# Optimization experiments

Hardware: AMD Instinct MI355X
Metric: run time of the kernel (lower is better)

## Reference

```python
import jax, jax.numpy as jnp
import numpy as np

B, SMAX, TMAX, D = 8, 4096, 4096, 528


def setup_inputs() -> dict:
    key = jax.random.key(0)
    ks = jax.random.split(key, 20)
    src_lens = (np.arange(B) * 256 + 2048).astype(np.int64)  # 2048..3840, sum 23552
    tgt_lens = (np.arange(B) * 224 + 2304).astype(np.int64)  # 2304..3872, sum 24704
    Ns, Nt = int(src_lens.sum()), int(tgt_lens.sum())
    N = Ns + Nt  # 48256 packed coarse points (src then tgt)
    src_mask = jnp.asarray(np.arange(SMAX)[None, :] < src_lens[:, None])
    tgt_mask = jnp.asarray(np.arange(TMAX)[None, :] < tgt_lens[:, None])
    sics = np.concatenate([b * SMAX + np.arange(l) for b, l in enumerate(src_lens)])
    tics = np.concatenate([b * TMAX + np.arange(l) for b, l in enumerate(tgt_lens)])
    w = lambda k, shape: (jax.random.normal(k, shape, jnp.float32) * 0.02)
    return dict(
        geo_feats=jax.random.normal(ks[0], (N, D), jnp.float32),
        pcd=jax.random.normal(ks[1], (N, 3), jnp.float32),
        Wi1=w(ks[2], (528, 528)), bi1=w(ks[3], (528,)),
        Wi2=w(ks[4], (1024, 528)), bi2=w(ks[5], (1024,)),
        Wc1=w(ks[6], (528, 528)), bc1=w(ks[7], (528,)),
        Wc2=w(ks[8], (1024, 528)), bc2=w(ks[9], (1024,)),
        Ws1=w(ks[10], (512, 2576)), bs1=w(ks[11], (512,)),
        Ws2=w(ks[12], (256, 512)), bs2=w(ks[13], (256,)),
        Ws3=w(ks[14], (1, 256)), bs3=w(ks[15], (1,)),
        src_mask=src_mask, tgt_mask=tgt_mask,
        src_ind_coarse_split=jnp.asarray(sics, jnp.int32),
        tgt_ind_coarse_split=jnp.asarray(tics, jnp.int32),
        src_ind_coarse=jnp.arange(Ns, dtype=jnp.int32),
        tgt_ind_coarse=Ns + jnp.arange(Nt, dtype=jnp.int32),
    )


def _scatter(vals, flat_idx, b, n, d):
    # split_feats: zeros[b*n, d]; out[flat_idx] = vals; view(b, n, d)
    return jnp.zeros((b * n, d), vals.dtype).at[flat_idx].set(vals).reshape(b, n, d)


def _pw(x, W, b):
    # pointwise Conv1d(in->out, k=1) as a batched matmul over positions
    return jnp.einsum('bnd,od->bno', x, W) + b


def reference(geo_feats, pcd, Wi1, bi1, Wi2, bi2, Wc1, bc1, Wc2, bc2,
              Ws1, bs1, Ws2, bs2, Ws3, bs3,
              src_mask, tgt_mask, src_ind_coarse_split, tgt_ind_coarse_split,
              src_ind_coarse, tgt_ind_coarse):
    b, smax = src_mask.shape
    tmax = tgt_mask.shape[1]
    d = geo_feats.shape[-1]

    # split_feats: ragged gather -> padded [B, pts_max, D]
    src_feats = _scatter(geo_feats[src_ind_coarse], src_ind_coarse_split, b, smax, d)
    tgt_feats = _scatter(geo_feats[tgt_ind_coarse], tgt_ind_coarse_split, b, tmax, d)
    s_pcd = _scatter(pcd[src_ind_coarse], src_ind_coarse_split, b, smax, 3)
    t_pcd = _scatter(pcd[tgt_ind_coarse], tgt_ind_coarse_split, b, tmax, 3)

    sm = src_mask.astype(src_feats.dtype)
    tm = tgt_mask.astype(tgt_feats.dtype)

    # inst_global over valid src points (per-sample slice -> masked mean)
    h = jax.nn.relu(_pw(src_feats, Wi1, bi1))
    h = jax.nn.relu(_pw(h, Wi2, bi2))                      # [B, Smax, 1024]
    inst_g = jnp.einsum('bno,bn->bo', h, sm) / sm.sum(1, keepdims=True)

    # category_global over valid tgt points
    g = jax.nn.relu(_pw(tgt_feats, Wc1, bc1))
    g = jax.nn.relu(_pw(g, Wc2, bc2))                      # [B, Tmax, 1024]
    cat_g = jnp.einsum('bno,bn->bo', g, tm) / tm.sum(1, keepdims=True)

    # scale_net on concat(src_feats, inst_g, cat_g) without materializing [B,N,2576]:
    # split first conv weight over the concat axis; globals contribute per-batch constants
    Ws1_s, Ws1_i, Ws1_c = Ws1[:, :d], Ws1[:, d:d + 1024], Ws1[:, d + 1024:]
    glob = inst_g @ Ws1_i.T + cat_g @ Ws1_c.T + bs1        # [B, 512]
    z = jax.nn.relu(jnp.einsum('bnd,od->bno', src_feats, Ws1_s) + glob[:, None, :])
    z = jax.nn.relu(_pw(z, Ws2, bs2))                      # [B, Smax, 256]
    s = _pw(z, Ws3, bs3)                                   # [B, Smax, 1]
    scale_mat = jax.nn.sigmoid(s).transpose(0, 2, 1) - 0.5  # [B, 1, Smax]

    inv = 1.0 / jnp.sqrt(jnp.asarray(d, src_feats.dtype))
    return (src_feats * inv, tgt_feats * inv, s_pcd, t_pcd, scale_mat)
```

## Files before the change

### kernel.cpp

```cpp
#include <hip/hip_runtime.h>
#include <hip/hip_bf16.h>
#include <cstdint>
#include <cstddef>

typedef float f32x4 __attribute__((ext_vector_type(4)));
typedef __bf16 bf16x8v __attribute__((ext_vector_type(8)));
typedef __hip_bfloat16 bf16;

__device__ __forceinline__ void gld16(const void* g, void* l) {
  __builtin_amdgcn_global_load_lds((const __attribute__((address_space(1))) void*)g,
                                   (__attribute__((address_space(3))) void*)l, 16, 0, 0);
}


struct PrepP {
  const float* Wsrc[6];
  bf16* Wdst[6];
  int sld[6], rows[6], K[6], Kpad[6];
  int off[10];
  float* zbuf; int ztotal;
  const float* geo; bf16* geo_b; int Nrows;
  const int* sics; const int* tics; int Ns, Nt; int* cnt;
};

__global__ void prep_kernel(PrepP P) {
  int blk = blockIdx.x;
  int job = 0;
  while (job < 8 && blk >= P.off[job + 1]) ++job;
  int local = blk - P.off[job];
  if (job < 6) {
    int i = local * 256 + threadIdx.x;
    int kp = P.Kpad[job];
    int total = P.rows[job] * kp;
    if (i < total) {
      int r = i / kp, k = i - r * kp;
      float v = (k < P.K[job]) ? P.Wsrc[job][(size_t)r * P.sld[job] + k] : 0.f;
      P.Wdst[job][i] = __float2bfloat16(v);
    }
  } else if (job == 6) {
    int i = local * 256 + threadIdx.x;
    if (i < P.ztotal) P.zbuf[i] = 0.f;
  } else if (job == 7) {
    int t = local * 256 + threadIdx.x;
    int row = t / 72, c8 = t - row * 72;
    if (row < P.Nrows) {
      int col = c8 * 8;
      bf16* dst = P.geo_b + (size_t)row * 576 + col;
      if (c8 < 66) {
        const float* s = P.geo + (size_t)row * 528 + col;
        float4 f0 = ((const float4*)s)[0], f1 = ((const float4*)s)[1];
        bf16 h[8] = {__float2bfloat16(f0.x), __float2bfloat16(f0.y),
                     __float2bfloat16(f0.z), __float2bfloat16(f0.w),
                     __float2bfloat16(f1.x), __float2bfloat16(f1.y),
                     __float2bfloat16(f1.z), __float2bfloat16(f1.w)};
        ((uint4*)dst)[0] = *(uint4*)h;
      } else {
        uint4 z = {0u, 0u, 0u, 0u};
        ((uint4*)dst)[0] = z;
      }
    }
  } else {
    int j = local * 256 + threadIdx.x;
    if (j < P.Ns) {
      if (j == 0) { P.cnt[0] = 0; P.cnt[8] = P.Ns; }
      else { int b = P.sics[j] >> 12; if ((P.sics[j - 1] >> 12) != b) P.cnt[b] = j; }
    }
    if (j < P.Nt) {
      if (j == 0) { P.cnt[9] = 0; P.cnt[17] = P.Nt; }
      else { int b = P.tics[j] >> 12; if ((P.tics[j - 1] >> 12) != b) P.cnt[9 + b] = j; }
    }
  }
}

__device__ __forceinline__ void gemm_core(
    const bf16* __restrict__ Aptr, int lda,
    const bf16* __restrict__ Bw, int ldb,
    int m0, int n0, int kiters,
    bf16* __restrict__ lA, bf16* __restrict__ lB,
    f32x4 acc[4][4])
{
  const int tid  = threadIdx.x;
  const int lane = tid & 63;
  const int quad = lane >> 4;
  const int l16  = lane & 15;
  const int wr   = tid >> 7;
  const int wc   = (tid >> 6) & 1;
  const int srow = tid >> 2;
  const int scol = (tid & 3) << 3;
  const bf16* aA0 = Aptr + (size_t)(m0 + srow) * lda + scol;
  const bf16* aA1 = aA0 + (size_t)64 * lda;
  const bf16* aB0 = Bw + (size_t)(n0 + srow) * ldb + scol;
  const bf16* aB1 = aB0 + (size_t)64 * ldb;
  bf16* lA00 = lA + tid * 8;        bf16* lA01 = lA + 2048 + tid * 8;
  bf16* lA10 = lA + 4096 + tid * 8; bf16* lA11 = lA + 6144 + tid * 8;
  bf16* lB00 = lB + tid * 8;        bf16* lB01 = lB + 2048 + tid * 8;
  bf16* lB10 = lB + 4096 + tid * 8; bf16* lB11 = lB + 6144 + tid * 8;

  for (int k = 0; k < kiters; ++k) {
    const int k0 = k * 64;
    gld16(aA0 + k0, lA00);      gld16(aA1 + k0, lA01);
    gld16(aA0 + k0 + 32, lA10); gld16(aA1 + k0 + 32, lA11);
    gld16(aB0 + k0, lB00);      gld16(aB1 + k0, lB01);
    gld16(aB0 + k0 + 32, lB10); gld16(aB1 + k0 + 32, lB11);
    __syncthreads();
#pragma unroll
    for (int kk = 0; kk < 2; ++kk) {
      bf16x8v af[4], bfr[4];
#pragma unroll
      for (int i = 0; i < 4; ++i) {
        af[i]  = *(const bf16x8v*)&lA[kk * 4096 + (wr * 64 + i * 16 + l16) * 32 + quad * 8];
        bfr[i] = *(const bf16x8v*)&lB[kk * 4096 + (wc * 64 + i * 16 + l16) * 32 + quad * 8];
      }
#pragma unroll
      for (int mi = 0; mi < 4; ++mi)
#pragma unroll
        for (int ni = 0; ni < 4; ++ni)
          acc[mi][ni] = __builtin_amdgcn_mfma_f32_16x16x32_bf16(af[mi], bfr[ni], acc[mi][ni], 0, 0, 0);
    }
    __syncthreads();
  }
}

__global__ __launch_bounds__(256, 2)
void kernelA(const bf16* __restrict__ geo_b,
             const bf16* __restrict__ Wi1b, const bf16* __restrict__ Wc1b,
             const bf16* __restrict__ Ws1sb,
             const float* __restrict__ bi1, const float* __restrict__ bc1,
             bf16* __restrict__ big_s, bf16* __restrict__ big_t,
             bf16* __restrict__ zpre, int Ms, int Mt)
{
  __shared__ alignas(16) bf16 lA[8192], lB[8192];
  const int x = blockIdx.x;
  const int e0 = Ms * 5, e1 = e0 + Mt * 5;
  const bf16 *A, *B; const float* bias = nullptr; bf16* out;
  int m0, n0, ldo, epi;
  if (x < e0) {
    int mt = x / 5, nt = x - mt * 5;
    m0 = mt * 128; n0 = nt * 128;
    A = geo_b; B = Wi1b; bias = bi1; out = big_s; ldo = 576; epi = 0;
  } else if (x < e1) {
    int y = x - e0; int mt = y / 5, nt = y - mt * 5;
    m0 = mt * 128; n0 = nt * 128;
    A = geo_b + (size_t)Ms * 128 * 576; B = Wc1b; bias = bc1; out = big_t; ldo = 576; epi = 0;
  } else {
    int y = x - e1; int mt = y / 4, nt = y - mt * 4;
    m0 = mt * 128; n0 = nt * 128;
    A = geo_b; B = Ws1sb; out = zpre; ldo = 512; epi = 1;
  }

  f32x4 acc[4][4];
  const f32x4 z4 = {0.f, 0.f, 0.f, 0.f};
#pragma unroll
  for (int i = 0; i < 4; ++i)
#pragma unroll
    for (int j = 0; j < 4; ++j) acc[i][j] = z4;

  gemm_core(A, 576, B, 576, m0, n0, 9, lA, lB, acc);

  const int lane = threadIdx.x & 63, quad = lane >> 4, l16 = lane & 15;
  const int wr = threadIdx.x >> 7, wc = (threadIdx.x >> 6) & 1;
#pragma unroll
  for (int mi = 0; mi < 4; ++mi) {
#pragma unroll
    for (int r = 0; r < 4; ++r) {
      const int row = m0 + wr * 64 + mi * 16 + quad * 4 + r;
#pragma unroll
      for (int ni = 0; ni < 4; ++ni) {
        const int col = n0 + wc * 64 + ni * 16 + l16;
        if (epi == 0) {
          if (col < 528)
            out[(size_t)row * ldo + col] = __float2bfloat16(fmaxf(acc[mi][ni][r] + bias[col], 0.f));
          else if (col < 576)
            out[(size_t)row * ldo + col] = __float2bfloat16(0.f);
        } else {
          out[(size_t)row * ldo + col] = __float2bfloat16(acc[mi][ni][r]);
        }
      }
    }
  }
}

__global__ __launch_bounds__(256, 2)
void kernelB(const bf16* __restrict__ big_s, const bf16* __restrict__ big_t,
             const bf16* __restrict__ Wi2b, const bf16* __restrict__ Wc2b,
             const float* __restrict__ bi2, const float* __restrict__ bc2,
             float* __restrict__ iacc, float* __restrict__ cacc,
             const int* __restrict__ sics, const int* __restrict__ tics,
             int Ms, int Mt,
             const float* __restrict__ geo, const float* __restrict__ pcd,
             const int* __restrict__ cnt,
             float* __restrict__ out0, float* __restrict__ out1,
             float* __restrict__ out2, float* __restrict__ out3,
             int Ns, float inv)
{
  __shared__ alignas(16) bf16 lA[8192], lB[8192];
  const int x = blockIdx.x;
  const int e0 = Ms * 8, e1 = e0 + Mt * 8;
  if (x >= e1) {
    int f = x - e1;
    int lane = threadIdx.x & 63;
    int rv = f * 4 + (threadIdx.x >> 6);
    bool is_t = rv >= 32768;
    int pos = is_t ? rv - 32768 : rv;
    int b = pos >> 12, r = pos & 4095;
    int base = is_t ? cnt[9 + b] : cnt[b];
    int lim  = (is_t ? cnt[9 + b + 1] : cnt[b + 1]) - base;
    float* op = (is_t ? out1 : out0) + (size_t)pos * 528;
    float* pp = (is_t ? out3 : out2) + (size_t)pos * 3;
    if (r < lim) {
      int sr = (is_t ? Ns : 0) + base + r;
      const float4* g = (const float4*)(geo + (size_t)sr * 528);
      for (int d = lane; d < 132; d += 64) {
        float4 v = g[d];
        float4 s = {v.x * inv, v.y * inv, v.z * inv, v.w * inv};
        ((float4*)op)[d] = s;
      }
      if (lane < 3) pp[lane] = pcd[(size_t)sr * 3 + lane];
    } else {
      float4 z = {0.f, 0.f, 0.f, 0.f};
      for (int d = lane; d < 132; d += 64) ((float4*)op)[d] = z;
      if (lane < 3) pp[lane] = 0.f;
    }
    return;
  }
  const bf16 *A, *B; const float* bias; float* red; const int* ridx;
  int m0, n0;
  if (x < e0) {
    int mt = x / 8, nt = x - mt * 8;
    m0 = mt * 128; n0 = nt * 128;
    A = big_s; B = Wi2b; bias = bi2; red = iacc; ridx = sics;
  } else {
    int y = x - e0; int mt = y / 8, nt = y - mt * 8;
    m0 = mt * 128; n0 = nt * 128;
    A = big_t; B = Wc2b; bias = bc2; red = cacc; ridx = tics;
  }

  f32x4 acc[4][4];
  const f32x4 z4 = {0.f, 0.f, 0.f, 0.f};
#pragma unroll
  for (int i = 0; i < 4; ++i)
#pragma unroll
    for (int j = 0; j < 4; ++j) acc[i][j] = z4;

  gemm_core(A, 576, B, 576, m0, n0, 9, lA, lB, acc);

  const int lane = threadIdx.x & 63, quad = lane >> 4, l16 = lane & 15;
  const int wr = threadIdx.x >> 7, wc = (threadIdx.x >> 6) & 1;
  const int b0r = ridx[m0] >> 12;
#pragma unroll
  for (int ni = 0; ni < 4; ++ni) {
    const int col = n0 + wc * 64 + ni * 16 + l16;
    const float bcol = bias[col];
#pragma unroll
    for (int mi = 0; mi < 4; ++mi) {
      float v0 = 0.f, v1 = 0.f;
#pragma unroll
      for (int r = 0; r < 4; ++r) {
        const int row = m0 + wr * 64 + mi * 16 + quad * 4 + r;
        const float v = fmaxf(acc[mi][ni][r] + bcol, 0.f);
        const int b = ridx[row] >> 12;
        if (b == b0r) v0 += v; else v1 += v;
      }
      v0 += __shfl_xor(v0, 16, 64); v0 += __shfl_xor(v0, 32, 64);
      v1 += __shfl_xor(v1, 16, 64); v1 += __shfl_xor(v1, 32, 64);
      if (quad == 0) {
        atomicAdd(&red[b0r * 1024 + col], v0);
        if (b0r + 1 < 8 && v1 != 0.f) atomicAdd(&red[(b0r + 1) * 1024 + col], v1);
      }
    }
  }
}

__global__ __launch_bounds__(256, 2)
void kernelC(const bf16* __restrict__ zpre, const bf16* __restrict__ Ws2b,
             const float* __restrict__ bs2, const float* __restrict__ Ws3,
             float* __restrict__ sbuf)
{
  __shared__ alignas(16) bf16 lA[8192], lB[8192];
  const int m0 = blockIdx.x * 128, n0 = blockIdx.y * 128;
  f32x4 acc[4][4];
  const f32x4 z4 = {0.f, 0.f, 0.f, 0.f};
#pragma unroll
  for (int i = 0; i < 4; ++i)
#pragma unroll
    for (int j = 0; j < 4; ++j) acc[i][j] = z4;

  gemm_core(zpre, 512, Ws2b, 512, m0, n0, 8, lA, lB, acc);

  const int lane = threadIdx.x & 63, quad = lane >> 4, l16 = lane & 15;
  const int wr = threadIdx.x >> 7, wc = (threadIdx.x >> 6) & 1;
#pragma unroll
  for (int mi = 0; mi < 4; ++mi) {
#pragma unroll
    for (int r = 0; r < 4; ++r) {
      const int row = m0 + wr * 64 + mi * 16 + quad * 4 + r;
      float p = 0.f;
#pragma unroll
      for (int ni = 0; ni < 4; ++ni) {
        const int col = n0 + wc * 64 + ni * 16 + l16;
        p += fmaxf(acc[mi][ni][r] + bs2[col], 0.f) * Ws3[col];
      }
      p += __shfl_xor(p, 1, 64); p += __shfl_xor(p, 2, 64);
      p += __shfl_xor(p, 4, 64); p += __shfl_xor(p, 8, 64);
      if (l16 == 0) atomicAdd(&sbuf[row], p);
    }
  }
}

__global__ __launch_bounds__(256) void glob_kernel(const float* __restrict__ iacc,
                                                   const float* __restrict__ cacc,
                                                   const int* __restrict__ cnt,
                                                   const float* __restrict__ Ws1,
                                                   const float* __restrict__ bs1,
                                                   float* __restrict__ globv) {
  int w    = (blockIdx.x * 256 + threadIdx.x) >> 6;
  int lane = threadIdx.x & 63;
  int b = w >> 9;
  int o = w & 511;
  const float* wi  = Ws1 + (size_t)o * 2576 + 528;
  const float* wcp = Ws1 + (size_t)o * 2576 + 1552;
  float a1 = 0.f, a2 = 0.f;
  for (int k = lane; k < 1024; k += 64) {
    a1 += iacc[b * 1024 + k] * wi[k];
    a2 += cacc[b * 1024 + k] * wcp[k];
  }
  for (int off = 32; off; off >>= 1) {
    a1 += __shfl_xor(a1, off, 64);
    a2 += __shfl_xor(a2, off, 64);
  }
  if (lane == 0) {
    float ns = (float)(cnt[b + 1] - cnt[b]);
    float nt = (float)(cnt[9 + b + 1] - cnt[9 + b]);
    globv[b * 512 + o] = bs1[o] + a1 / ns + a2 / nt;
  }
}

__global__ __launch_bounds__(256) void s_empty_kernel(const float* __restrict__ globv,
                                                      const float* __restrict__ Ws2,
                                                      const float* __restrict__ bs2,
                                                      const float* __restrict__ Ws3,
                                                      const float* __restrict__ bs3,
                                                      float* __restrict__ semp) {
  __shared__ float zrow[512];
  __shared__ float wsum[4];
  int b = blockIdx.x, t = threadIdx.x;
  zrow[t]       = fmaxf(globv[b * 512 + t], 0.f);
  zrow[t + 256] = fmaxf(globv[b * 512 + t + 256], 0.f);
  __syncthreads();
  float acc = bs2[t];
  for (int o = 0; o < 512; ++o) acc += zrow[o] * Ws2[t * 512 + o];
  float p = fmaxf(acc, 0.f) * Ws3[t];
  for (int off = 32; off; off >>= 1) p += __shfl_xor(p, off, 64);
  if ((t & 63) == 0) wsum[t >> 6] = p;
  __syncthreads();
  if (t == 0) semp[b] = wsum[0] + wsum[1] + wsum[2] + wsum[3] + bs3[0];
}

__global__ void zfix_kernel(bf16* __restrict__ z, const float* __restrict__ globv,
                            const int* __restrict__ sics, int total) {
  int idx = blockIdx.x * 256 + threadIdx.x;
  if (idx >= total) return;
  int row = idx >> 6, c0 = (idx & 63) << 3;
  int b = sics[row] >> 12;
  const float* gv = globv + b * 512 + c0;
  bf16* zp = z + (size_t)row * 512 + c0;
  uint4 u = *(uint4*)zp;
  bf16* e = (bf16*)&u;
#pragma unroll
  for (int i = 0; i < 8; ++i)
    e[i] = __float2bfloat16(fmaxf(__bfloat162float(e[i]) + gv[i], 0.f));
  *(uint4*)zp = u;
}

__global__ void scale_kernel(const float* __restrict__ sbuf,
                             const float* __restrict__ semp,
                             const int* __restrict__ cnt,
                             const float* __restrict__ bs3,
                             float* __restrict__ out4) {
  int i = blockIdx.x * 256 + threadIdx.x;
  if (i >= 32768) return;
  int b = i >> 12, r = i & 4095;
  int base = cnt[b];
  int lim = cnt[b + 1] - base;
  float s = (r < lim) ? sbuf[base + r] + bs3[0] : semp[b];
  out4[i] = 1.f / (1.f + expf(-s)) - 0.5f;
}


extern "C" void kernel_launch(void* const* d_in, const int* in_sizes, int n_in,
                              void* d_out, int out_size, void* d_ws, size_t ws_size,
                              hipStream_t stream) {
  const float* geo = (const float*)d_in[0];
  const float* pcd = (const float*)d_in[1];
  const float* Wi1 = (const float*)d_in[2];
  const float* bi1 = (const float*)d_in[3];
  const float* Wi2 = (const float*)d_in[4];
  const float* bi2 = (const float*)d_in[5];
  const float* Wc1 = (const float*)d_in[6];
  const float* bc1 = (const float*)d_in[7];
  const float* Wc2 = (const float*)d_in[8];
  const float* bc2 = (const float*)d_in[9];
  const float* Ws1 = (const float*)d_in[10];
  const float* bs1 = (const float*)d_in[11];
  const float* Ws2 = (const float*)d_in[12];
  const float* bs2 = (const float*)d_in[13];
  const float* Ws3 = (const float*)d_in[14];
  const float* bs3 = (const float*)d_in[15];
  const int* sics = (const int*)d_in[18];
  const int* tics = (const int*)d_in[19];
  const int Ns = in_sizes[18];
  const int Nt = in_sizes[19];
  const int Ms = Ns / 128, Mt = Nt / 128;
  const int Nrows = Ns + Nt;

  float* out0 = (float*)d_out;
  float* out1 = out0 + (size_t)8 * 4096 * 528;
  float* out2 = out1 + (size_t)8 * 4096 * 528;
  float* out3 = out2 + (size_t)8 * 4096 * 3;
  float* out4 = out3 + (size_t)8 * 4096 * 3;

  char* wp = (char*)d_ws;
  auto alloc = [&](size_t bytes) -> void* {
    void* p = (void*)wp;
    wp += (bytes + 255) & ~(size_t)255;
    return p;
  };
  int*   cnt   = (int*)  alloc(128);
  float* iacc  = (float*)alloc((size_t)8 * 1024 * 4);
  float* cacc  = (float*)alloc((size_t)8 * 1024 * 4);
  float* sbuf  = (float*)alloc((size_t)Ns * 4);
  float* globb = (float*)alloc((size_t)8 * 512 * 4);
  float* semp  = (float*)alloc(64);
  bf16* Wi1b  = (bf16*)alloc((size_t)640  * 576 * 2);
  bf16* Wi2b  = (bf16*)alloc((size_t)1024 * 576 * 2);
  bf16* Wc1b  = (bf16*)alloc((size_t)640  * 576 * 2);
  bf16* Wc2b  = (bf16*)alloc((size_t)1024 * 576 * 2);
  bf16* Ws1sb = (bf16*)alloc((size_t)512  * 576 * 2);
  bf16* Ws2b  = (bf16*)alloc((size_t)256  * 512 * 2);
  bf16* geo_b = (bf16*)alloc((size_t)Nrows * 576 * 2);
  bf16* big_s = (bf16*)alloc((size_t)Ns * 576 * 2);
  bf16* big_t = (bf16*)alloc((size_t)Nt * 576 * 2);
  bf16* zpre  = (bf16*)alloc((size_t)Ns * 512 * 2);

  PrepP P;
  {
    const float* srcs[6] = {Wi1, Wi2, Wc1, Wc2, Ws1, Ws2};
    bf16* dsts[6]        = {Wi1b, Wi2b, Wc1b, Wc2b, Ws1sb, Ws2b};
    int slds[6] = {528, 528, 528, 528, 2576, 512};
    int rows[6] = {528, 1024, 528, 1024, 512, 256};
    int Ks[6]   = {528, 528, 528, 528, 528, 512};
    int Kps[6]  = {576, 576, 576, 576, 576, 512};
    int nblk = 0;
    for (int i = 0; i < 6; ++i) {
      P.Wsrc[i] = srcs[i]; P.Wdst[i] = dsts[i]; P.sld[i] = slds[i];
      P.rows[i] = rows[i]; P.K[i] = Ks[i]; P.Kpad[i] = Kps[i];
      P.off[i] = nblk;
      nblk += (rows[i] * Kps[i] + 255) / 256;
    }
    P.off[6] = nblk;
    P.zbuf = iacc; P.ztotal = 8192 + 8192 + Ns;
    nblk += (P.ztotal + 255) / 256;
    P.off[7] = nblk;
    P.geo = geo; P.geo_b = geo_b; P.Nrows = Nrows;
    nblk += ((Nrows * 72) + 255) / 256;
    P.off[8] = nblk;
    P.sics = sics; P.tics = tics; P.Ns = Ns; P.Nt = Nt; P.cnt = cnt;
    int n = Ns > Nt ? Ns : Nt;
    nblk += (n + 255) / 256;
    P.off[9] = nblk;
    prep_kernel<<<dim3(nblk), dim3(256), 0, stream>>>(P);
  }

  kernelA<<<dim3(Ms * 5 + Mt * 5 + Ms * 4), dim3(256), 0, stream>>>(
      geo_b, Wi1b, Wc1b, Ws1sb, bi1, bc1, big_s, big_t, zpre, Ms, Mt);

  float inv = 1.0f / sqrtf(528.0f);
  kernelB<<<dim3(Ms * 8 + Mt * 8 + 16384), dim3(256), 0, stream>>>(
      big_s, big_t, Wi2b, Wc2b, bi2, bc2, iacc, cacc, sics, tics, Ms, Mt,
      geo, pcd, cnt, out0, out1, out2, out3, Ns, inv);

  glob_kernel<<<dim3(1024), dim3(256), 0, stream>>>(iacc, cacc, cnt, Ws1, bs1, globb);
  s_empty_kernel<<<dim3(8), dim3(256), 0, stream>>>(globb, Ws2, bs2, Ws3, bs3, semp);
  zfix_kernel<<<dim3((Ns * 64 + 255) / 256), dim3(256), 0, stream>>>(zpre, globb, sics, Ns * 64);
  kernelC<<<dim3(Ms, 2), dim3(256), 0, stream>>>(zpre, Ws2b, bs2, Ws3, sbuf);
  scale_kernel<<<dim3(128), dim3(256), 0, stream>>>(sbuf, semp, cnt, bs3, out4);
}
```

Before: 518.2 us.

## Fuse scaled-feature scatter into prep pass and add XCD-aware block swizzle

Moves the scaled feature and point-cloud scatter out of kernelB's extra blocks into the prep kernel's bf16 conversion pass. geo is now read once for both the bf16 copy and the scaled fp32 output, and only padding rows are zeroed, found by binary search. It also remaps block indices in kernelA, kernelB and kernelC so consecutive tiles stay on the same XCD for L2 reuse. The cost is an index lookup per prep thread and somewhat scattered writes.

```diff
diff --git a/kernel.cpp b/kernel.cpp
--- a/kernel.cpp
+++ b/kernel.cpp
@@ -12,21 +12,35 @@
                                    (__attribute__((address_space(3))) void*)l, 16, 0, 0);
 }
 
+__device__ __forceinline__ int xcd_swz(int orig, int nwg) {
+  int q = nwg >> 3, r = nwg & 7;
+  int x = orig & 7, i = orig >> 3;
+  return (x < r ? x * (q + 1) : r * (q + 1) + (x - r) * q) + i;
+}
+
+__device__ __forceinline__ int lbound(const int* a, int n, int v) {
+  int lo = 0, hi = n;
+  while (lo < hi) { int m = (lo + hi) >> 1; if (a[m] < v) lo = m + 1; else hi = m; }
+  return lo;
+}
+
 
 struct PrepP {
   const float* Wsrc[6];
   bf16* Wdst[6];
   int sld[6], rows[6], K[6], Kpad[6];
-  int off[10];
+  int off[11];
   float* zbuf; int ztotal;
   const float* geo; bf16* geo_b; int Nrows;
+  const float* pcd;
+  float* out0; float* out1; float* out2; float* out3; float inv;
   const int* sics; const int* tics; int Ns, Nt; int* cnt;
 };
 
 __global__ void prep_kernel(PrepP P) {
   int blk = blockIdx.x;
   int job = 0;
-  while (job < 8 && blk >= P.off[job + 1]) ++job;
+  while (job < 9 && blk >= P.off[job + 1]) ++job;
   int local = blk - P.off[job];
   if (job < 6) {
     int i = local * 256 + threadIdx.x;
@@ -44,6 +58,8 @@
     int t = local * 256 + threadIdx.x;
     int row = t / 72, c8 = t - row * 72;
     if (row < P.Nrows) {
+      bool is_t = row >= P.Ns;
+      int pos = is_t ? P.tics[row - P.Ns] : P.sics[row];
       int col = c8 * 8;
       bf16* dst = P.geo_b + (size_t)row * 576 + col;
       if (c8 < 66) {
@@ -54,12 +70,21 @@
                      __float2bfloat16(f1.x), __float2bfloat16(f1.y),
                      __float2bfloat16(f1.z), __float2bfloat16(f1.w)};
         ((uint4*)dst)[0] = *(uint4*)h;
+        float* op = (is_t ? P.out1 : P.out0) + (size_t)pos * 528 + col;
+        float4 s0 = {f0.x * P.inv, f0.y * P.inv, f0.z * P.inv, f0.w * P.inv};
+        float4 s1 = {f1.x * P.inv, f1.y * P.inv, f1.z * P.inv, f1.w * P.inv};
+        ((float4*)op)[0] = s0;
+        ((float4*)op)[1] = s1;
       } else {
         uint4 z = {0u, 0u, 0u, 0u};
         ((uint4*)dst)[0] = z;
+        if (c8 < 69) {
+          int j = c8 - 66;
+          (is_t ? P.out3 : P.out2)[(size_t)pos * 3 + j] = P.pcd[(size_t)row * 3 + j];
+        }
       }
     }
-  } else {
+  } else if (job == 8) {
     int j = local * 256 + threadIdx.x;
     if (j < P.Ns) {
       if (j == 0) { P.cnt[0] = 0; P.cnt[8] = P.Ns; }
@@ -68,6 +93,22 @@
     if (j < P.Nt) {
       if (j == 0) { P.cnt[9] = 0; P.cnt[17] = P.Nt; }
       else { int b = P.tics[j] >> 12; if ((P.tics[j - 1] >> 12) != b) P.cnt[9 + b] = j; }
+    }
+  } else {
+    int lane = threadIdx.x & 63;
+    int rv = local * 4 + (threadIdx.x >> 6);
+    bool is_t = rv >= 32768;
+    int pos = is_t ? rv - 32768 : rv;
+    int b = pos >> 12, r = pos & 4095;
+    const int* arr = is_t ? P.tics : P.sics;
+    int n = is_t ? P.Nt : P.Ns;
+    int lo = lbound(arr, n, b << 12);
+    int hi = lbound(arr, n, (b + 1) << 12);
+    if (r >= hi - lo) {
+      float* op = (is_t ? P.out1 : P.out0) + (size_t)pos * 528;
+      float4 z = {0.f, 0.f, 0.f, 0.f};
+      for (int d = lane; d < 132; d += 64) ((float4*)op)[d] = z;
+      if (lane < 3) (is_t ? P.out3 : P.out2)[(size_t)pos * 3 + lane] = 0.f;
     }
   }
 }
@@ -130,7 +171,7 @@
              bf16* __restrict__ zpre, int Ms, int Mt)
 {
   __shared__ alignas(16) bf16 lA[8192], lB[8192];
-  const int x = blockIdx.x;
+  const int x = xcd_swz(blockIdx.x, gridDim.x);
   const int e0 = Ms * 5, e1 = e0 + Mt * 5;
   const bf16 *A, *B; const float* bias = nullptr; bf16* out;
   int m0, n0, ldo, epi;
@@ -186,43 +227,11 @@
              const float* __restrict__ bi2, const float* __restrict__ bc2,
              float* __restrict__ iacc, float* __restrict__ cacc,
              const int* __restrict__ sics, const int* __restrict__ tics,
-             int Ms, int Mt,
-             const float* __restrict__ geo, const float* __restrict__ pcd,
-             const int* __restrict__ cnt,
-             float* __restrict__ out0, float* __restrict__ out1,
-             float* __restrict__ out2, float* __restrict__ out3,
-             int Ns, float inv)
+             int Ms, int Mt)
 {
   __shared__ alignas(16) bf16 lA[8192], lB[8192];
-  const int x = blockIdx.x;
-  const int e0 = Ms * 8, e1 = e0 + Mt * 8;
-  if (x >= e1) {
-    int f = x - e1;
-    int lane = threadIdx.x & 63;
-    int rv = f * 4 + (threadIdx.x >> 6);
-    bool is_t = rv >= 32768;
-    int pos = is_t ? rv - 32768 : rv;
-    int b = pos >> 12, r = pos & 4095;
-    int base = is_t ? cnt[9 + b] : cnt[b];
-    int lim  = (is_t ? cnt[9 + b + 1] : cnt[b + 1]) - base;
-    float* op = (is_t ? out1 : out0) + (size_t)pos * 528;
-    float* pp = (is_t ? out3 : out2) + (size_t)pos * 3;
-    if (r < lim) {
-      int sr = (is_t ? Ns : 0) + base + r;
-      const float4* g = (const float4*)(geo + (size_t)sr * 528);
-      for (int d = lane; d < 132; d += 64) {
-        float4 v = g[d];
-        float4 s = {v.x * inv, v.y * inv, v.z * inv, v.w * inv};
-        ((float4*)op)[d] = s;
-      }
-      if (lane < 3) pp[lane] = pcd[(size_t)sr * 3 + lane];
-    } else {
-      float4 z = {0.f, 0.f, 0.f, 0.f};
-      for (int d = lane; d < 132; d += 64) ((float4*)op)[d] = z;
-      if (lane < 3) pp[lane] = 0.f;
-    }
-    return;
-  }
+  const int x = xcd_swz(blockIdx.x, gridDim.x);
+  const int e0 = Ms * 8;
   const bf16 *A, *B; const float* bias; float* red; const int* ridx;
   int m0, n0;
   if (x < e0) {
@@ -277,7 +286,8 @@
              float* __restrict__ sbuf)
 {
   __shared__ alignas(16) bf16 lA[8192], lB[8192];
-  const int m0 = blockIdx.x * 128, n0 = blockIdx.y * 128;
+  const int x = xcd_swz(blockIdx.x, gridDim.x);
+  const int m0 = (x >> 1) * 128, n0 = (x & 1) * 128;
   f32x4 acc[4][4];
   const f32x4 z4 = {0.f, 0.f, 0.f, 0.f};
 #pragma unroll
@@ -442,6 +452,8 @@
   bf16* big_t = (bf16*)alloc((size_t)Nt * 576 * 2);
   bf16* zpre  = (bf16*)alloc((size_t)Ns * 512 * 2);
 
+  float inv = 1.0f / sqrtf(528.0f);
+
   PrepP P;
   {
     const float* srcs[6] = {Wi1, Wi2, Wc1, Wc2, Ws1, Ws2};
@@ -462,26 +474,28 @@
     nblk += (P.ztotal + 255) / 256;
     P.off[7] = nblk;
     P.geo = geo; P.geo_b = geo_b; P.Nrows = Nrows;
+    P.pcd = pcd;
+    P.out0 = out0; P.out1 = out1; P.out2 = out2; P.out3 = out3; P.inv = inv;
     nblk += ((Nrows * 72) + 255) / 256;
     P.off[8] = nblk;
     P.sics = sics; P.tics = tics; P.Ns = Ns; P.Nt = Nt; P.cnt = cnt;
     int n = Ns > Nt ? Ns : Nt;
     nblk += (n + 255) / 256;
     P.off[9] = nblk;
+    nblk += 65536 / 4;
+    P.off[10] = nblk;
     prep_kernel<<<dim3(nblk), dim3(256), 0, stream>>>(P);
   }
 
   kernelA<<<dim3(Ms * 5 + Mt * 5 + Ms * 4), dim3(256), 0, stream>>>(
       geo_b, Wi1b, Wc1b, Ws1sb, bi1, bc1, big_s, big_t, zpre, Ms, Mt);
 
-  float inv = 1.0f / sqrtf(528.0f);
-  kernelB<<<dim3(Ms * 8 + Mt * 8 + 16384), dim3(256), 0, stream>>>(
-      big_s, big_t, Wi2b, Wc2b, bi2, bc2, iacc, cacc, sics, tics, Ms, Mt,
-      geo, pcd, cnt, out0, out1, out2, out3, Ns, inv);
+  kernelB<<<dim3(Ms * 8 + Mt * 8), dim3(256), 0, stream>>>(
+      big_s, big_t, Wi2b, Wc2b, bi2, bc2, iacc, cacc, sics, tics, Ms, Mt);
 
   glob_kernel<<<dim3(1024), dim3(256), 0, stream>>>(iacc, cacc, cnt, Ws1, bs1, globb);
   s_empty_kernel<<<dim3(8), dim3(256), 0, stream>>>(globb, Ws2, bs2, Ws3, bs3, semp);
   zfix_kernel<<<dim3((Ns * 64 + 255) / 256), dim3(256), 0, stream>>>(zpre, globb, sics, Ns * 64);
-  kernelC<<<dim3(Ms, 2), dim3(256), 0, stream>>>(zpre, Ws2b, bs2, Ws3, sbuf);
+  kernelC<<<dim3(Ms * 2), dim3(256), 0, stream>>>(zpre, Ws2b, bs2, Ws3, sbuf);
   scale_kernel<<<dim3(128), dim3(256), 0, stream>>>(sbuf, semp, cnt, bs3, out4);
 }
```

After: 526.0 us. No clear change (+1.5%).

## Move feature copy into first GEMM kernel interleaved, add XCD-aware block swizzle

Applied to the files above, without the earlier changes.

Moves the memory-bound output copy/scale blocks from kernelB into kernelA and interleaves them with the GEMM tiles, one GEMM block for every six copy blocks, so bandwidth-bound work overlaps compute-bound work. Adds an XCD-aware block index remap to kernelA, kernelB and kernelC so that neighbouring tiles sharing operands land on the same XCD's L2. kernelC switches from a 2D grid to a 1D grid so the swizzle can apply. This may cost some GEMM tile throughput from contention with the copy blocks and adds index arithmetic.

```diff
diff --git a/kernel.cpp b/kernel.cpp
--- a/kernel.cpp
+++ b/kernel.cpp
@@ -10,6 +10,12 @@
 __device__ __forceinline__ void gld16(const void* g, void* l) {
   __builtin_amdgcn_global_load_lds((const __attribute__((address_space(1))) void*)g,
                                    (__attribute__((address_space(3))) void*)l, 16, 0, 0);
+}
+
+__device__ __forceinline__ int xcd_swz(int orig, int nwg) {
+  int q = nwg >> 3, r = nwg & 7;
+  int x = orig & 7, i = orig >> 3;
+  return (x < r ? x * (q + 1) : r * (q + 1) + (x - r) * q) + i;
 }
 
 
@@ -127,66 +133,7 @@
              const bf16* __restrict__ Ws1sb,
              const float* __restrict__ bi1, const float* __restrict__ bc1,
              bf16* __restrict__ big_s, bf16* __restrict__ big_t,
-             bf16* __restrict__ zpre, int Ms, int Mt)
-{
-  __shared__ alignas(16) bf16 lA[8192], lB[8192];
-  const int x = blockIdx.x;
-  const int e0 = Ms * 5, e1 = e0 + Mt * 5;
-  const bf16 *A, *B; const float* bias = nullptr; bf16* out;
-  int m0, n0, ldo, epi;
-  if (x < e0) {
-    int mt = x / 5, nt = x - mt * 5;
-    m0 = mt * 128; n0 = nt * 128;
-    A = geo_b; B = Wi1b; bias = bi1; out = big_s; ldo = 576; epi = 0;
-  } else if (x < e1) {
-    int y = x - e0; int mt = y / 5, nt = y - mt * 5;
-    m0 = mt * 128; n0 = nt * 128;
-    A = geo_b + (size_t)Ms * 128 * 576; B = Wc1b; bias = bc1; out = big_t; ldo = 576; epi = 0;
-  } else {
-    int y = x - e1; int mt = y / 4, nt = y - mt * 4;
-    m0 = mt * 128; n0 = nt * 128;
-    A = geo_b; B = Ws1sb; out = zpre; ldo = 512; epi = 1;
-  }
-
-  f32x4 acc[4][4];
-  const f32x4 z4 = {0.f, 0.f, 0.f, 0.f};
-#pragma unroll
-  for (int i = 0; i < 4; ++i)
-#pragma unroll
-    for (int j = 0; j < 4; ++j) acc[i][j] = z4;
-
-  gemm_core(A, 576, B, 576, m0, n0, 9, lA, lB, acc);
-
-  const int lane = threadIdx.x & 63, quad = lane >> 4, l16 = lane & 15;
-  const int wr = threadIdx.x >> 7, wc = (threadIdx.x >> 6) & 1;
-#pragma unroll
-  for (int mi = 0; mi < 4; ++mi) {
-#pragma unroll
-    for (int r = 0; r < 4; ++r) {
-      const int row = m0 + wr * 64 + mi * 16 + quad * 4 + r;
-#pragma unroll
-      for (int ni = 0; ni < 4; ++ni) {
-        const int col = n0 + wc * 64 + ni * 16 + l16;
-        if (epi == 0) {
-          if (col < 528)
-            out[(size_t)row * ldo + col] = __float2bfloat16(fmaxf(acc[mi][ni][r] + bias[col], 0.f));
-          else if (col < 576)
-            out[(size_t)row * ldo + col] = __float2bfloat16(0.f);
-        } else {
-          out[(size_t)row * ldo + col] = __float2bfloat16(acc[mi][ni][r]);
-        }
-      }
-    }
-  }
-}
-
-__global__ __launch_bounds__(256, 2)
-void kernelB(const bf16* __restrict__ big_s, const bf16* __restrict__ big_t,
-             const bf16* __restrict__ Wi2b, const bf16* __restrict__ Wc2b,
-             const float* __restrict__ bi2, const float* __restrict__ bc2,
-             float* __restrict__ iacc, float* __restrict__ cacc,
-             const int* __restrict__ sics, const int* __restrict__ tics,
-             int Ms, int Mt,
+             bf16* __restrict__ zpre, int Ms, int Mt,
              const float* __restrict__ geo, const float* __restrict__ pcd,
              const int* __restrict__ cnt,
              float* __restrict__ out0, float* __restrict__ out1,
@@ -194,10 +141,17 @@
              int Ns, float inv)
 {
   __shared__ alignas(16) bf16 lA[8192], lB[8192];
-  const int x = blockIdx.x;
-  const int e0 = Ms * 8, e1 = e0 + Mt * 8;
-  if (x >= e1) {
-    int f = x - e1;
+  const int nG = Ms * 5 + Mt * 5 + Ms * 4;
+  const int xb = blockIdx.x;
+  int x = -1, f = -1;
+  if (xb < 7 * nG) {
+    if (xb % 7 == 0) x = xb / 7;
+    else f = xb - xb / 7 - 1;
+  } else {
+    f = xb - nG;
+  }
+
+  if (x < 0) {
     int lane = threadIdx.x & 63;
     int rv = f * 4 + (threadIdx.x >> 6);
     bool is_t = rv >= 32768;
@@ -223,6 +177,68 @@
     }
     return;
   }
+
+  x = xcd_swz(x, nG);
+  const int e0 = Ms * 5, e1 = e0 + Mt * 5;
+  const bf16 *A, *B; const float* bias = nullptr; bf16* out;
+  int m0, n0, ldo, epi;
+  if (x < e0) {
+    int mt = x / 5, nt = x - mt * 5;
+    m0 = mt * 128; n0 = nt * 128;
+    A = geo_b; B = Wi1b; bias = bi1; out = big_s; ldo = 576; epi = 0;
+  } else if (x < e1) {
+    int y = x - e0; int mt = y / 5, nt = y - mt * 5;
+    m0 = mt * 128; n0 = nt * 128;
+    A = geo_b + (size_t)Ms * 128 * 576; B = Wc1b; bias = bc1; out = big_t; ldo = 576; epi = 0;
+  } else {
+    int y = x - e1; int mt = y / 4, nt = y - mt * 4;
+    m0 = mt * 128; n0 = nt * 128;
+    A = geo_b; B = Ws1sb; out = zpre; ldo = 512; epi = 1;
+  }
+
+  f32x4 acc[4][4];
+  const f32x4 z4 = {0.f, 0.f, 0.f, 0.f};
+#pragma unroll
+  for (int i = 0; i < 4; ++i)
+#pragma unroll
+    for (int j = 0; j < 4; ++j) acc[i][j] = z4;
+
+  gemm_core(A, 576, B, 576, m0, n0, 9, lA, lB, acc);
+
+  const int lane = threadIdx.x & 63, quad = lane >> 4, l16 = lane & 15;
+  const int wr = threadIdx.x >> 7, wc = (threadIdx.x >> 6) & 1;
+#pragma unroll
+  for (int mi = 0; mi < 4; ++mi) {
+#pragma unroll
+    for (int r = 0; r < 4; ++r) {
+      const int row = m0 + wr * 64 + mi * 16 + quad * 4 + r;
+#pragma unroll
+      for (int ni = 0; ni < 4; ++ni) {
+        const int col = n0 + wc * 64 + ni * 16 + l16;
+        if (epi == 0) {
+          if (col < 528)
+            out[(size_t)row * ldo + col] = __float2bfloat16(fmaxf(acc[mi][ni][r] + bias[col], 0.f));
+          else if (col < 576)
+            out[(size_t)row * ldo + col] = __float2bfloat16(0.f);
+        } else {
+          out[(size_t)row * ldo + col] = __float2bfloat16(acc[mi][ni][r]);
+        }
+      }
+    }
+  }
+}
+
+__global__ __launch_bounds__(256, 2)
+void kernelB(const bf16* __restrict__ big_s, const bf16* __restrict__ big_t,
+             const bf16* __restrict__ Wi2b, const bf16* __restrict__ Wc2b,
+             const float* __restrict__ bi2, const float* __restrict__ bc2,
+             float* __restrict__ iacc, float* __restrict__ cacc,
+             const int* __restrict__ sics, const int* __restrict__ tics,
+             int Ms, int Mt)
+{
+  __shared__ alignas(16) bf16 lA[8192], lB[8192];
+  const int x = xcd_swz(blockIdx.x, gridDim.x);
+  const int e0 = Ms * 8;
   const bf16 *A, *B; const float* bias; float* red; const int* ridx;
   int m0, n0;
   if (x < e0) {
@@ -277,7 +293,8 @@
              float* __restrict__ sbuf)
 {
   __shared__ alignas(16) bf16 lA[8192], lB[8192];
-  const int m0 = blockIdx.x * 128, n0 = blockIdx.y * 128;
+  const int x = xcd_swz(blockIdx.x, gridDim.x);
+  const int m0 = (x >> 1) * 128, n0 = (x & 1) * 128;
   f32x4 acc[4][4];
   const f32x4 z4 = {0.f, 0.f, 0.f, 0.f};
 #pragma unroll
@@ -442,6 +459,8 @@
   bf16* big_t = (bf16*)alloc((size_t)Nt * 576 * 2);
   bf16* zpre  = (bf16*)alloc((size_t)Ns * 512 * 2);
 
+  float inv = 1.0f / sqrtf(528.0f);
+
   PrepP P;
   {
     const float* srcs[6] = {Wi1, Wi2, Wc1, Wc2, Ws1, Ws2};
@@ -471,17 +490,20 @@
     prep_kernel<<<dim3(nblk), dim3(256), 0, stream>>>(P);
   }
 
-  kernelA<<<dim3(Ms * 5 + Mt * 5 + Ms * 4), dim3(256), 0, stream>>>(
-      geo_b, Wi1b, Wc1b, Ws1sb, bi1, bc1, big_s, big_t, zpre, Ms, Mt);
-
-  float inv = 1.0f / sqrtf(528.0f);
-  kernelB<<<dim3(Ms * 8 + Mt * 8 + 16384), dim3(256), 0, stream>>>(
-      big_s, big_t, Wi2b, Wc2b, bi2, bc2, iacc, cacc, sics, tics, Ms, Mt,
-      geo, pcd, cnt, out0, out1, out2, out3, Ns, inv);
+  {
+    const int nG = Ms * 5 + Mt * 5 + Ms * 4;
+    const int nF = 16384;
+    kernelA<<<dim3(nG + nF), dim3(256), 0, stream>>>(
+        geo_b, Wi1b, Wc1b, Ws1sb, bi1, bc1, big_s, big_t, zpre, Ms, Mt,
+        geo, pcd, cnt, out0, out1, out2, out3, Ns, inv);
+  }
+
+  kernelB<<<dim3(Ms * 8 + Mt * 8), dim3(256), 0, stream>>>(
+      big_s, big_t, Wi2b, Wc2b, bi2, bc2, iacc, cacc, sics, tics, Ms, Mt);
 
   glob_kernel<<<dim3(1024), dim3(256), 0, stream>>>(iacc, cacc, cnt, Ws1, bs1, globb);
   s_empty_kernel<<<dim3(8), dim3(256), 0, stream>>>(globb, Ws2, bs2, Ws3, bs3, semp);
   zfix_kernel<<<dim3((Ns * 64 + 255) / 256), dim3(256), 0, stream>>>(zpre, globb, sics, Ns * 64);
-  kernelC<<<dim3(Ms, 2), dim3(256), 0, stream>>>(zpre, Ws2b, bs2, Ws3, sbuf);
+  kernelC<<<dim3(Ms * 2), dim3(256), 0, stream>>>(zpre, Ws2b, bs2, Ws3, sbuf);
   scale_kernel<<<dim3(128), dim3(256), 0, stream>>>(sbuf, semp, cnt, bs3, out4);
 }
```

New measurement: 534.1 us. 3.1% more time.

## Fuse zfix into kernelC A-staging, add XCD block swizzle, coalesce s_empty

Applied to the files above, without the earlier changes.

Removes the separate zfix pass over zpre by applying the per-batch global bias and ReLU while staging A tiles into LDS inside kernelC. That saves one read and one write of the Ns×512 bf16 buffer, at the cost of staging A through registers instead of direct global-to-LDS loads. Adds an XCD-aware block index swizzle to kernelA, kernelB (GEMM part) and kernelC so that neighbouring tiles land on the same XCD and share L2. It also rewrites s_empty_kernel so each wave reduces rows with coalesced weight reads.

```diff
diff --git a/kernel.cpp b/kernel.cpp
--- a/kernel.cpp
+++ b/kernel.cpp
@@ -10,6 +10,12 @@
 __device__ __forceinline__ void gld16(const void* g, void* l) {
   __builtin_amdgcn_global_load_lds((const __attribute__((address_space(1))) void*)g,
                                    (__attribute__((address_space(3))) void*)l, 16, 0, 0);
+}
+
+__device__ __forceinline__ int xcd_swz(int orig, int nwg) {
+  int q = nwg >> 3, r = nwg & 7;
+  int x = orig & 7, i = orig >> 3;
+  return (x < r ? x * (q + 1) : r * (q + 1) + (x - r) * q) + i;
 }
 
 
@@ -130,7 +136,7 @@
              bf16* __restrict__ zpre, int Ms, int Mt)
 {
   __shared__ alignas(16) bf16 lA[8192], lB[8192];
-  const int x = blockIdx.x;
+  const int x = xcd_swz(blockIdx.x, gridDim.x);
   const int e0 = Ms * 5, e1 = e0 + Mt * 5;
   const bf16 *A, *B; const float* bias = nullptr; bf16* out;
   int m0, n0, ldo, epi;
@@ -194,10 +200,10 @@
              int Ns, float inv)
 {
   __shared__ alignas(16) bf16 lA[8192], lB[8192];
-  const int x = blockIdx.x;
+  const int xb = blockIdx.x;
   const int e0 = Ms * 8, e1 = e0 + Mt * 8;
-  if (x >= e1) {
-    int f = x - e1;
+  if (xb >= e1) {
+    int f = xb - e1;
     int lane = threadIdx.x & 63;
     int rv = f * 4 + (threadIdx.x >> 6);
     bool is_t = rv >= 32768;
@@ -223,6 +229,7 @@
     }
     return;
   }
+  const int x = xcd_swz(xb, e1);
   const bf16 *A, *B; const float* bias; float* red; const int* ridx;
   int m0, n0;
   if (x < e0) {
@@ -274,10 +281,28 @@
 __global__ __launch_bounds__(256, 2)
 void kernelC(const bf16* __restrict__ zpre, const bf16* __restrict__ Ws2b,
              const float* __restrict__ bs2, const float* __restrict__ Ws3,
+             const float* __restrict__ globv, const int* __restrict__ sics,
              float* __restrict__ sbuf)
 {
   __shared__ alignas(16) bf16 lA[8192], lB[8192];
-  const int m0 = blockIdx.x * 128, n0 = blockIdx.y * 128;
+  const int x = xcd_swz(blockIdx.x, gridDim.x);
+  const int m0 = (x >> 1) * 128, n0 = (x & 1) * 128;
+  const int tid  = threadIdx.x;
+  const int lane = tid & 63, quad = lane >> 4, l16 = lane & 15;
+  const int wr = tid >> 7, wc = (tid >> 6) & 1;
+  const int srow = tid >> 2;
+  const int scol = (tid & 3) << 3;
+
+  const int r0g = m0 + srow, r1g = r0g + 64;
+  const float* gv0 = globv + ((size_t)(sics[r0g] >> 12) << 9);
+  const float* gv1 = globv + ((size_t)(sics[r1g] >> 12) << 9);
+  const bf16* za0 = zpre + (size_t)r0g * 512 + scol;
+  const bf16* za1 = zpre + (size_t)r1g * 512 + scol;
+  const bf16* aB0 = Ws2b + (size_t)(n0 + srow) * 512 + scol;
+  const bf16* aB1 = aB0 + (size_t)64 * 512;
+  bf16* lB00 = lB + tid * 8;        bf16* lB01 = lB + 2048 + tid * 8;
+  bf16* lB10 = lB + 4096 + tid * 8; bf16* lB11 = lB + 6144 + tid * 8;
+
   f32x4 acc[4][4];
   const f32x4 z4 = {0.f, 0.f, 0.f, 0.f};
 #pragma unroll
@@ -285,10 +310,42 @@
 #pragma unroll
     for (int j = 0; j < 4; ++j) acc[i][j] = z4;
 
-  gemm_core(zpre, 512, Ws2b, 512, m0, n0, 8, lA, lB, acc);
-
-  const int lane = threadIdx.x & 63, quad = lane >> 4, l16 = lane & 15;
-  const int wr = threadIdx.x >> 7, wc = (threadIdx.x >> 6) & 1;
+  auto stageA = [&](const bf16* src, const float* gv, int col, bf16* dst) {
+    uint4 u = *(const uint4*)src;
+    bf16 e[8]; *(uint4*)e = u;
+    bf16 o[8];
+#pragma unroll
+    for (int i = 0; i < 8; ++i)
+      o[i] = __float2bfloat16(fmaxf(__bfloat162float(e[i]) + gv[col + i], 0.f));
+    *(uint4*)dst = *(uint4*)o;
+  };
+
+  for (int k = 0; k < 8; ++k) {
+    const int k0 = k * 64;
+    gld16(aB0 + k0, lB00);      gld16(aB1 + k0, lB01);
+    gld16(aB0 + k0 + 32, lB10); gld16(aB1 + k0 + 32, lB11);
+    stageA(za0 + k0,      gv0, k0 + scol,      lA + tid * 8);
+    stageA(za1 + k0,      gv1, k0 + scol,      lA + 2048 + tid * 8);
+    stageA(za0 + k0 + 32, gv0, k0 + scol + 32, lA + 4096 + tid * 8);
+    stageA(za1 + k0 + 32, gv1, k0 + scol + 32, lA + 6144 + tid * 8);
+    __syncthreads();
+#pragma unroll
+    for (int kk = 0; kk < 2; ++kk) {
+      bf16x8v af[4], bfr[4];
+#pragma unroll
+      for (int i = 0; i < 4; ++i) {
+        af[i]  = *(const bf16x8v*)&lA[kk * 4096 + (wr * 64 + i * 16 + l16) * 32 + quad * 8];
+        bfr[i] = *(const bf16x8v*)&lB[kk * 4096 + (wc * 64 + i * 16 + l16) * 32 + quad * 8];
+      }
+#pragma unroll
+      for (int mi = 0; mi < 4; ++mi)
+#pragma unroll
+        for (int ni = 0; ni < 4; ++ni)
+          acc[mi][ni] = __builtin_amdgcn_mfma_f32_16x16x32_bf16(af[mi], bfr[ni], acc[mi][ni], 0, 0, 0);
+    }
+    __syncthreads();
+  }
+
 #pragma unroll
   for (int mi = 0; mi < 4; ++mi) {
 #pragma unroll
@@ -347,29 +404,21 @@
   zrow[t]       = fmaxf(globv[b * 512 + t], 0.f);
   zrow[t + 256] = fmaxf(globv[b * 512 + t + 256], 0.f);
   __syncthreads();
-  float acc = bs2[t];
-  for (int o = 0; o < 512; ++o) acc += zrow[o] * Ws2[t * 512 + o];
-  float p = fmaxf(acc, 0.f) * Ws3[t];
-  for (int off = 32; off; off >>= 1) p += __shfl_xor(p, off, 64);
-  if ((t & 63) == 0) wsum[t >> 6] = p;
+  int w = t >> 6, lane = t & 63;
+  float ws = 0.f;
+  for (int tt = w * 64; tt < w * 64 + 64; ++tt) {
+    float a = 0.f;
+#pragma unroll
+    for (int oi = 0; oi < 8; ++oi) {
+      int o = lane + oi * 64;
+      a += zrow[o] * Ws2[(size_t)tt * 512 + o];
+    }
+    for (int off = 32; off; off >>= 1) a += __shfl_xor(a, off, 64);
+    if (lane == 0) ws += fmaxf(a + bs2[tt], 0.f) * Ws3[tt];
+  }
+  if (lane == 0) wsum[w] = ws;
   __syncthreads();
   if (t == 0) semp[b] = wsum[0] + wsum[1] + wsum[2] + wsum[3] + bs3[0];
-}
-
-__global__ void zfix_kernel(bf16* __restrict__ z, const float* __restrict__ globv,
-                            const int* __restrict__ sics, int total) {
-  int idx = blockIdx.x * 256 + threadIdx.x;
-  if (idx >= total) return;
-  int row = idx >> 6, c0 = (idx & 63) << 3;
-  int b = sics[row] >> 12;
-  const float* gv = globv + b * 512 + c0;
-  bf16* zp = z + (size_t)row * 512 + c0;
-  uint4 u = *(uint4*)zp;
-  bf16* e = (bf16*)&u;
-#pragma unroll
-  for (int i = 0; i < 8; ++i)
-    e[i] = __float2bfloat16(fmaxf(__bfloat162float(e[i]) + gv[i], 0.f));
-  *(uint4*)zp = u;
 }
 
 __global__ void scale_kernel(const float* __restrict__ sbuf,
@@ -442,6 +491,8 @@
   bf16* big_t = (bf16*)alloc((size_t)Nt * 576 * 2);
   bf16* zpre  = (bf16*)alloc((size_t)Ns * 512 * 2);
 
+  float inv = 1.0f / sqrtf(528.0f);
+
   PrepP P;
   {
     const float* srcs[6] = {Wi1, Wi2, Wc1, Wc2, Ws1, Ws2};
@@ -474,14 +525,12 @@
   kernelA<<<dim3(Ms * 5 + Mt * 5 + Ms * 4), dim3(256), 0, stream>>>(
       geo_b, Wi1b, Wc1b, Ws1sb, bi1, bc1, big_s, big_t, zpre, Ms, Mt);
 
-  float inv = 1.0f / sqrtf(528.0f);
   kernelB<<<dim3(Ms * 8 + Mt * 8 + 16384), dim3(256), 0, stream>>>(
       big_s, big_t, Wi2b, Wc2b, bi2, bc2, iacc, cacc, sics, tics, Ms, Mt,
       geo, pcd, cnt, out0, out1, out2, out3, Ns, inv);
 
   glob_kernel<<<dim3(1024), dim3(256), 0, stream>>>(iacc, cacc, cnt, Ws1, bs1, globb);
   s_empty_kernel<<<dim3(8), dim3(256), 0, stream>>>(globb, Ws2, bs2, Ws3, bs3, semp);
-  zfix_kernel<<<dim3((Ns * 64 + 255) / 256), dim3(256), 0, stream>>>(zpre, globb, sics, Ns * 64);
-  kernelC<<<dim3(Ms, 2), dim3(256), 0, stream>>>(zpre, Ws2b, bs2, Ws3, sbuf);
+  kernelC<<<dim3(Ms * 2), dim3(256), 0, stream>>>(zpre, Ws2b, bs2, Ws3, globb, sics, sbuf);
   scale_kernel<<<dim3(128), dim3(256), 0, stream>>>(sbuf, semp, cnt, bs3, out4);
 }
```

Measured after the change: 536.5 us. 1.04x slower.
